# Optimization experiments

Hardware: AMD Instinct MI355X
Metric: run time of the kernel (lower is better)

The kernel has to match this reference:

```python
import jax, jax.numpy as jnp
import numpy as np

HEADS = 4
DIM_HEAD = 64


def setup_inputs() -> dict:
    key = jax.random.key(0)
    k1, k2, k3, k4 = jax.random.split(key, 4)
    dim = 256
    hidden = HEADS * DIM_HEAD  # 256
    x = jax.random.normal(k1, (16, dim, 64, 64), dtype=jnp.float32)
    # 1x1 conv weights stored as [out_c, in_c]
    w_qkv = jax.random.normal(k2, (3 * hidden, dim), dtype=jnp.float32) * (1.0 / np.sqrt(dim))
    w_out = jax.random.normal(k3, (dim, hidden), dtype=jnp.float32) * (1.0 / np.sqrt(hidden))
    b_out = jax.random.normal(k4, (dim,), dtype=jnp.float32) * 0.01
    gamma = jnp.ones((dim,), dtype=jnp.float32) * 1e-05
    return {"x": x, "w_qkv": w_qkv, "w_out": w_out, "b_out": b_out, "gamma": gamma}


def reference(x, w_qkv, w_out, b_out, gamma):
    b, c, h, w = x.shape
    n = h * w
    # 1x1 conv == channel matmul
    qkv = jnp.einsum('oc,bchw->bohw', w_qkv, x)  # [b, 3*heads*dh, h, w]
    qkv = qkv.reshape(b, 3, HEADS, DIM_HEAD, n)  # channel split order: (qkv, heads, c)
    q, k, v = qkv[:, 0], qkv[:, 1], qkv[:, 2]    # each [b, heads, dh, n]
    k = jax.nn.softmax(k, axis=-1)               # softmax over spatial tokens
    context = jnp.einsum('bhdn,bhen->bhde', k, v)  # [b, heads, dh, dh]
    out = jnp.einsum('bhde,bhdn->bhen', context, q)  # [b, heads, dh, n]
    out = out.reshape(b, HEADS * DIM_HEAD, h, w)
    y = jnp.einsum('oc,bchw->bohw', w_out, out) + b_out[None, :, None, None]
    return y * gamma[None, :, None, None] + x
```

## Files before the change

kernel.cpp:

```cpp
#include <hip/hip_runtime.h>
#include <stdint.h>

typedef short s16x8 __attribute__((ext_vector_type(8)));
typedef float f32x4 __attribute__((ext_vector_type(4)));
typedef unsigned int u32x2 __attribute__((ext_vector_type(2)));

typedef const __attribute__((address_space(1))) void glb_cv;
typedef __attribute__((address_space(3))) void lds_v;

__device__ __forceinline__ float bits2f(unsigned short u) {
    union { unsigned int i; float f; } c; c.i = ((unsigned int)u) << 16; return c.f;
}
__device__ __forceinline__ unsigned short f2bits(float f) {
    union { float f; unsigned int i; } c; c.f = f;
    unsigned int x = c.i;
    unsigned int r = (x + 0x7FFFu + ((x >> 16) & 1u)) >> 16;
    return (unsigned short)r;
}
__device__ __forceinline__ unsigned int pack2(float a, float b) {
    return (unsigned int)f2bits(a) | ((unsigned int)f2bits(b) << 16);
}

__device__ __forceinline__ void gl_lds16(const void* g, void* l) {
    __builtin_amdgcn_global_load_lds((glb_cv*)g, (lds_v*)l, 16, 0, 0);
}

__global__ __launch_bounds__(256) void k_cvt(
    const float* __restrict__ src, unsigned short* __restrict__ dst, int n8)
{
    int i = blockIdx.x * 256 + threadIdx.x;
    if (i >= n8) return;
    const float* s = src + (size_t)i * 8;
    float4 a = *(const float4*)s, b = *(const float4*)(s + 4);
    unsigned int q[4] = { pack2(a.x, a.y), pack2(a.z, a.w), pack2(b.x, b.y), pack2(b.z, b.w) };
    *(s16x8*)(dst + (size_t)i * 8) = *(s16x8*)q;
}

__global__ __launch_bounds__(256) void k_transpose(
    const unsigned short* __restrict__ src, unsigned short* __restrict__ dst,
    int RS, int DS)
{
    int dr = blockIdx.x * 256 + threadIdx.x;
    int c0 = blockIdx.y * 8;
    __align__(16) unsigned short tmp[8];
#pragma unroll
    for (int j = 0; j < 8; ++j) tmp[j] = src[(size_t)(c0 + j) * RS + dr];
    *(s16x8*)(dst + (size_t)dr * DS + c0) = *(s16x8*)tmp;
}

__global__ __launch_bounds__(256) void k_prepw(
    const float* __restrict__ wqkv, const float* __restrict__ wout,
    unsigned short* __restrict__ wb, unsigned short* __restrict__ wob,
    unsigned short* __restrict__ WqT)
{
    int i = blockIdx.x * 256 + threadIdx.x;
    if (i < 32768) {
        const float* s; unsigned short* d; int j;
        if (i < 24576) { s = wqkv; d = wb; j = i; }
        else           { s = wout; d = wob; j = i - 24576; }
        const float* sp = s + (size_t)j * 8;
        float4 a = *(const float4*)sp, b = *(const float4*)(sp + 4);
        unsigned int q[4] = { pack2(a.x, a.y), pack2(a.z, a.w), pack2(b.x, b.y), pack2(b.z, b.w) };
        *(s16x8*)(d + (size_t)j * 8) = *(s16x8*)q;
    } else {
        int j = i - 32768;
        int dr = j & 255, c0 = (j >> 8) * 8;
        __align__(16) unsigned short tmp[8];
#pragma unroll
        for (int jj = 0; jj < 8; ++jj)
            tmp[jj] = f2bits(wqkv[(size_t)(c0 + jj) * 256 + dr]);
        *(s16x8*)(WqT + (size_t)dr * 256 + c0) = *(s16x8*)tmp;
    }
}

__global__ __launch_bounds__(256) void k_prep(
    const float* __restrict__ x, unsigned short* __restrict__ xT,
    unsigned short* __restrict__ xbf)
{
    __shared__ unsigned short Ts[64][264];
    int b = blockIdx.y, n0 = blockIdx.x * 64, t = threadIdx.x;
    const float* xb = x + (size_t)b * 1048576;
    unsigned short* xbfb = xbf + (size_t)b * 1048576;
#pragma unroll
    for (int i = 0; i < 16; ++i) {
        int idx = t + i * 256;
        int c = idx >> 4, nq = idx & 15;
        float4 v = *(const float4*)(xb + (size_t)c * 4096 + n0 + nq * 4);
        u32x2 q; q[0] = pack2(v.x, v.y); q[1] = pack2(v.z, v.w);
        *(u32x2*)(xbfb + (size_t)c * 4096 + n0 + nq * 4) = q;
        float vv[4] = { v.x, v.y, v.z, v.w };
#pragma unroll
        for (int e = 0; e < 4; ++e) {
            int ee = (e + c) & 3;
            Ts[nq * 4 + ee][c] = f2bits(vv[ee]);
        }
    }
    __syncthreads();
    unsigned short* xTb = xT + (size_t)b * 1048576 + (size_t)n0 * 256;
#pragma unroll
    for (int i = 0; i < 8; ++i) {
        int idx = t + i * 256;
        int nl = idx >> 5, cg = (idx & 31) * 8;
        *(s16x8*)(xTb + (size_t)nl * 256 + cg) = *(const s16x8*)&Ts[nl][cg];
    }
}

template <int EPI>
__global__ __launch_bounds__(256) void gemm_bt2(
    const unsigned short* __restrict__ A, const unsigned short* __restrict__ Bt,
    void* __restrict__ C,
    int K, int Kstep, int lda, int ldb, int ldc,
    long Abs, long Bbs, long Cbs,
    const float* __restrict__ Xres,
    const float* __restrict__ gamma,
    const float* __restrict__ bias)
{
    __shared__ __align__(16) unsigned short As[128 * 64];
    __shared__ __align__(16) unsigned short Bs[128 * 64];
    int bz = blockIdx.z;
    int b = bz & 15, kc = bz >> 4;
    int m0 = blockIdx.y * 128, n0 = blockIdx.x * 128;
    const unsigned short* Ab = A + (size_t)b * Abs + (size_t)m0 * lda + (size_t)kc * Kstep;
    const unsigned short* Bb = Bt + (size_t)b * Bbs + (size_t)n0 * ldb + (size_t)kc * Kstep;
    int t = threadIdx.x;
    int w = t >> 6, l = t & 63, lm = l & 15, lq = l >> 4;
    int mw = (w >> 1) * 64, nw = (w & 1) * 64;

    f32x4 acc[4][4];
    f32x4 zero = {0.f, 0.f, 0.f, 0.f};
#pragma unroll
    for (int i = 0; i < 4; ++i)
#pragma unroll
        for (int j = 0; j < 4; ++j) acc[i][j] = zero;

    for (int kk = 0; kk < K; kk += 64) {
#pragma unroll
        for (int i = 0; i < 4; ++i) {
            int idx = t + i * 256;
            int r = idx >> 3;
            int sch = (idx & 7) ^ (r & 7);
            int lbase = (i * 256 + w * 64) * 8;
            gl_lds16(Ab + (size_t)r * lda + kk + sch * 8, &As[lbase]);
            gl_lds16(Bb + (size_t)r * ldb + kk + sch * 8, &Bs[lbase]);
        }
        __syncthreads();
#pragma unroll
        for (int ks = 0; ks < 2; ++ks) {
            s16x8 af[4], bfr[4];
#pragma unroll
            for (int mi = 0; mi < 4; ++mi) {
                int row = mw + mi * 16 + lm;
                af[mi] = *(const s16x8*)&As[row * 64 + (((ks * 4 + lq) ^ (row & 7)) << 3)];
            }
#pragma unroll
            for (int ni = 0; ni < 4; ++ni) {
                int row = nw + ni * 16 + lm;
                bfr[ni] = *(const s16x8*)&Bs[row * 64 + (((ks * 4 + lq) ^ (row & 7)) << 3)];
            }
#pragma unroll
            for (int mi = 0; mi < 4; ++mi)
#pragma unroll
                for (int ni = 0; ni < 4; ++ni)
                    acc[mi][ni] = __builtin_amdgcn_mfma_f32_16x16x32_bf16(af[mi], bfr[ni], acc[mi][ni], 0, 0, 0);
        }
        __syncthreads();
    }

    if (EPI == 0) {
        unsigned short* Cb = (unsigned short*)C + (size_t)bz * Cbs;
#pragma unroll
        for (int mi = 0; mi < 4; ++mi)
#pragma unroll
            for (int r = 0; r < 4; ++r) {
                int m = m0 + mw + mi * 16 + lq * 4 + r;
#pragma unroll
                for (int ni = 0; ni < 4; ++ni) {
                    int n = n0 + nw + ni * 16 + lm;
                    Cb[(size_t)m * ldc + n] = f2bits(acc[mi][ni][r]);
                }
            }
    } else {
        float* Cb = (float*)C + (size_t)bz * Cbs;
        const float* Xb = Xres + (size_t)bz * Cbs;
#pragma unroll
        for (int mi = 0; mi < 4; ++mi)
#pragma unroll
            for (int r = 0; r < 4; ++r) {
                int m = m0 + mw + mi * 16 + lq * 4 + r;
                float g = gamma[m], bo = bias[m];
#pragma unroll
                for (int ni = 0; ni < 4; ++ni) {
                    int n = n0 + nw + ni * 16 + lm;
                    size_t idx = (size_t)m * ldc + n;
                    Cb[idx] = g * (acc[mi][ni][r] + bo) + Xb[idx];
                }
            }
    }
}

__global__ __launch_bounds__(256) void gemm64(
    const unsigned short* __restrict__ A, const unsigned short* __restrict__ Bt,
    unsigned short* __restrict__ C,
    int K, int Kstep, int lda, int ldb, int ldc,
    long Abs, long Bbs, long Cbs)
{
    __shared__ __align__(16) unsigned short As[64 * 64];
    __shared__ __align__(16) unsigned short Bs[64 * 64];
    int bz = blockIdx.z;
    int b = bz & 15, kc = bz >> 4;
    int m0 = blockIdx.y * 64, n0 = blockIdx.x * 64;
    const unsigned short* Ab = A + (size_t)b * Abs + (size_t)m0 * lda + (size_t)kc * Kstep;
    const unsigned short* Bb = Bt + (size_t)b * Bbs + (size_t)n0 * ldb + (size_t)kc * Kstep;
    int t = threadIdx.x;
    int w = t >> 6, l = t & 63, lm = l & 15, lq = l >> 4;
    int mw = (w >> 1) * 32, nw = (w & 1) * 32;

    f32x4 acc[2][2];
    f32x4 zero = {0.f, 0.f, 0.f, 0.f};
#pragma unroll
    for (int i = 0; i < 2; ++i)
#pragma unroll
        for (int j = 0; j < 2; ++j) acc[i][j] = zero;

    for (int kk = 0; kk < K; kk += 64) {
#pragma unroll
        for (int i = 0; i < 2; ++i) {
            int idx = t + i * 256;
            int r = idx >> 3;
            int sch = (idx & 7) ^ (r & 7);
            int lbase = (i * 256 + w * 64) * 8;
            gl_lds16(Ab + (size_t)r * lda + kk + sch * 8, &As[lbase]);
            gl_lds16(Bb + (size_t)r * ldb + kk + sch * 8, &Bs[lbase]);
        }
        __syncthreads();
#pragma unroll
        for (int ks = 0; ks < 2; ++ks) {
            s16x8 af[2], bfr[2];
#pragma unroll
            for (int mi = 0; mi < 2; ++mi) {
                int row = mw + mi * 16 + lm;
                af[mi] = *(const s16x8*)&As[row * 64 + (((ks * 4 + lq) ^ (row & 7)) << 3)];
            }
#pragma unroll
            for (int ni = 0; ni < 2; ++ni) {
                int row = nw + ni * 16 + lm;
                bfr[ni] = *(const s16x8*)&Bs[row * 64 + (((ks * 4 + lq) ^ (row & 7)) << 3)];
            }
#pragma unroll
            for (int mi = 0; mi < 2; ++mi)
#pragma unroll
                for (int ni = 0; ni < 2; ++ni)
                    acc[mi][ni] = __builtin_amdgcn_mfma_f32_16x16x32_bf16(af[mi], bfr[ni], acc[mi][ni], 0, 0, 0);
        }
        __syncthreads();
    }

    unsigned short* Cb = C + (size_t)bz * Cbs;
#pragma unroll
    for (int mi = 0; mi < 2; ++mi)
#pragma unroll
        for (int r = 0; r < 4; ++r) {
            int m = m0 + mw + mi * 16 + lq * 4 + r;
#pragma unroll
            for (int ni = 0; ni < 2; ++ni) {
                int n = n0 + nw + ni * 16 + lm;
                Cb[(size_t)m * ldc + n] = f2bits(acc[mi][ni][r]);
            }
        }
}

template <int BF32, int EPI>
__global__ __launch_bounds__(256) void gemm_bt(
    const unsigned short* __restrict__ A, const void* __restrict__ Bt,
    void* __restrict__ C,
    int K, int Kstep, int lda, int ldb, int ldc,
    long Abs, long Bbs, long Cbs,
    const float* __restrict__ Xres,
    const float* __restrict__ gamma,
    const float* __restrict__ bias)
{
    __shared__ unsigned short As[128][72];
    __shared__ unsigned short Bs[128][72];
    int bz = blockIdx.z;
    int b = bz & 15, kc = bz >> 4;
    int m0 = blockIdx.y * 128, n0 = blockIdx.x * 128;
    const unsigned short* Ab = A + (size_t)b * Abs + (size_t)m0 * lda + (size_t)kc * Kstep;
    size_t boff = (size_t)b * Bbs + (size_t)n0 * ldb + (size_t)kc * Kstep;
    int t = threadIdx.x;
    int w = t >> 6, l = t & 63, lm = l & 15, lq = l >> 4;
    int mw = (w >> 1) * 64, nw = (w & 1) * 64;

    f32x4 acc[4][4];
    f32x4 zero = {0.f, 0.f, 0.f, 0.f};
#pragma unroll
    for (int i = 0; i < 4; ++i)
#pragma unroll
        for (int j = 0; j < 4; ++j) acc[i][j] = zero;

    for (int kk = 0; kk < K; kk += 64) {
#pragma unroll
        for (int i = 0; i < 4; ++i) {
            int idx = t + i * 256;
            int r = idx >> 3, ch = idx & 7;
            *(s16x8*)&As[r][ch * 8] = *(const s16x8*)(Ab + (size_t)r * lda + kk + ch * 8);
            if (BF32) {
                const float* bp = (const float*)Bt + boff + (size_t)r * ldb + kk + ch * 8;
                float4 v0 = *(const float4*)bp, v1 = *(const float4*)(bp + 4);
                unsigned int q[4] = { pack2(v0.x, v0.y), pack2(v0.z, v0.w),
                                      pack2(v1.x, v1.y), pack2(v1.z, v1.w) };
                *(s16x8*)&Bs[r][ch * 8] = *(s16x8*)q;
            } else {
                const unsigned short* bp = (const unsigned short*)Bt + boff + (size_t)r * ldb + kk + ch * 8;
                *(s16x8*)&Bs[r][ch * 8] = *(const s16x8*)bp;
            }
        }
        __syncthreads();
#pragma unroll
        for (int ks = 0; ks < 2; ++ks) {
            s16x8 af[4], bfr[4];
#pragma unroll
            for (int mi = 0; mi < 4; ++mi) af[mi]  = *(const s16x8*)&As[mw + mi * 16 + lm][ks * 32 + lq * 8];
#pragma unroll
            for (int ni = 0; ni < 4; ++ni) bfr[ni] = *(const s16x8*)&Bs[nw + ni * 16 + lm][ks * 32 + lq * 8];
#pragma unroll
            for (int mi = 0; mi < 4; ++mi)
#pragma unroll
                for (int ni = 0; ni < 4; ++ni)
                    acc[mi][ni] = __builtin_amdgcn_mfma_f32_16x16x32_bf16(af[mi], bfr[ni], acc[mi][ni], 0, 0, 0);
        }
        __syncthreads();
    }

    if (EPI == 0) {
        unsigned short* Cb = (unsigned short*)C + (size_t)bz * Cbs;
#pragma unroll
        for (int mi = 0; mi < 4; ++mi)
#pragma unroll
            for (int r = 0; r < 4; ++r) {
                int m = m0 + mw + mi * 16 + lq * 4 + r;
#pragma unroll
                for (int ni = 0; ni < 4; ++ni) {
                    int n = n0 + nw + ni * 16 + lm;
                    Cb[(size_t)m * ldc + n] = f2bits(acc[mi][ni][r]);
                }
            }
    } else {
        float* Cb = (float*)C + (size_t)bz * Cbs;
        const float* Xb = Xres + (size_t)bz * Cbs;
#pragma unroll
        for (int mi = 0; mi < 4; ++mi)
#pragma unroll
            for (int r = 0; r < 4; ++r) {
                int m = m0 + mw + mi * 16 + lq * 4 + r;
                float g = gamma[m], bo = bias[m];
#pragma unroll
                for (int ni = 0; ni < 4; ++ni) {
                    int n = n0 + nw + ni * 16 + lm;
                    size_t idx = (size_t)m * ldc + n;
                    Cb[idx] = g * (acc[mi][ni][r] + bo) + Xb[idx];
                }
            }
    }
}

template <int EPI>
__global__ __launch_bounds__(256) void gemm_bn(
    const unsigned short* __restrict__ A, const float* __restrict__ B,
    void* __restrict__ C,
    int K, int lda, int ldb, int ldc,
    long Abs, long Bbs, long Cbs,
    const float* __restrict__ Xres,
    const float* __restrict__ gamma,
    const float* __restrict__ bias)
{
    __shared__ unsigned short As[128][72];
    __shared__ unsigned short Bs[64][130];
    int bz = blockIdx.z;
    int m0 = blockIdx.y * 128, n0 = blockIdx.x * 128;
    const unsigned short* Ab = A + (size_t)bz * Abs + (size_t)m0 * lda;
    const float* Bb = B + (size_t)bz * Bbs + n0;
    int t = threadIdx.x;
    int w = t >> 6, l = t & 63, lm = l & 15, lq = l >> 4;
    int mw = (w >> 1) * 64, nw = (w & 1) * 64;

    f32x4 acc[4][4];
    f32x4 zero = {0.f, 0.f, 0.f, 0.f};
#pragma unroll
    for (int i = 0; i < 4; ++i)
#pragma unroll
        for (int j = 0; j < 4; ++j) acc[i][j] = zero;

    for (int kk = 0; kk < K; kk += 64) {
#pragma unroll
        for (int i = 0; i < 4; ++i) {
            int idx = t + i * 256;
            int r = idx >> 3, ch = idx & 7;
            *(s16x8*)&As[r][ch * 8] = *(const s16x8*)(Ab + (size_t)r * lda + kk + ch * 8);
        }
#pragma unroll
        for (int i = 0; i < 4; ++i) {
            int idx = t + i * 256;
            int c = idx >> 4, cc = idx & 15;
            const float* bp = Bb + (size_t)(kk + c) * ldb + cc * 8;
            float4 v0 = *(const float4*)bp, v1 = *(const float4*)(bp + 4);
            unsigned int* q = (unsigned int*)&Bs[c][cc * 8];
            q[0] = pack2(v0.x, v0.y); q[1] = pack2(v0.z, v0.w);
            q[2] = pack2(v1.x, v1.y); q[3] = pack2(v1.z, v1.w);
        }
        __syncthreads();
#pragma unroll
        for (int ks = 0; ks < 2; ++ks) {
            s16x8 af[4];
#pragma unroll
            for (int mi = 0; mi < 4; ++mi) af[mi] = *(const s16x8*)&As[mw + mi * 16 + lm][ks * 32 + lq * 8];
#pragma unroll
            for (int ni = 0; ni < 4; ++ni) {
                s16x8 bfr;
#pragma unroll
                for (int j = 0; j < 8; ++j) bfr[j] = (short)Bs[ks * 32 + lq * 8 + j][nw + ni * 16 + lm];
#pragma unroll
                for (int mi = 0; mi < 4; ++mi)
                    acc[mi][ni] = __builtin_amdgcn_mfma_f32_16x16x32_bf16(af[mi], bfr, acc[mi][ni], 0, 0, 0);
            }
        }
        __syncthreads();
    }

#pragma unroll
    for (int mi = 0; mi < 4; ++mi)
#pragma unroll
        for (int r = 0; r < 4; ++r) {
            int m = m0 + mw + mi * 16 + lq * 4 + r;
            float g = 0.f, bo = 0.f;
            if (EPI == 1) { g = gamma[m]; bo = bias[m]; }
#pragma unroll
            for (int ni = 0; ni < 4; ++ni) {
                int n = n0 + nw + ni * 16 + lm;
                size_t idx = (size_t)m * ldc + n;
                float v = acc[mi][ni][r];
                if (EPI == 1) {
                    float* Cb = (float*)C + (size_t)bz * Cbs;
                    Cb[idx] = g * (v + bo) + Xres[(size_t)bz * Cbs + idx];
                } else {
                    unsigned short* Cb = (unsigned short*)C + (size_t)bz * Cbs;
                    Cb[idx] = f2bits(v);
                }
            }
        }
}

__global__ __launch_bounds__(256) void k_softmax(unsigned short* __restrict__ kbuf)
{
    unsigned short* p = kbuf + (size_t)blockIdx.x * 4096;
    int t = threadIdx.x;
    __shared__ float red[4];

    s16x8 r0 = *(const s16x8*)(p + t * 16);
    s16x8 r1 = *(const s16x8*)(p + t * 16 + 8);
    float v[16];
    float m = -1e30f;
#pragma unroll
    for (int i = 0; i < 8; ++i) { v[i] = bits2f((unsigned short)r0[i]); v[8 + i] = bits2f((unsigned short)r1[i]); }
#pragma unroll
    for (int i = 0; i < 16; ++i) m = fmaxf(m, v[i]);
#pragma unroll
    for (int off = 32; off >= 1; off >>= 1) m = fmaxf(m, __shfl_xor(m, off));
    if ((t & 63) == 0) red[t >> 6] = m;
    __syncthreads();
    m = fmaxf(fmaxf(red[0], red[1]), fmaxf(red[2], red[3]));
    __syncthreads();

    float s = 0.f;
#pragma unroll
    for (int i = 0; i < 16; ++i) { v[i] = __expf(v[i] - m); s += v[i]; }
#pragma unroll
    for (int off = 32; off >= 1; off >>= 1) s += __shfl_xor(s, off);
    if ((t & 63) == 0) red[t >> 6] = s;
    __syncthreads();
    s = red[0] + red[1] + red[2] + red[3];
    float inv = 1.0f / s;

    __align__(16) unsigned short otmp[16];
#pragma unroll
    for (int i = 0; i < 16; ++i) otmp[i] = f2bits(v[i] * inv);
    *(s16x8*)(p + t * 16) = *(s16x8*)(otmp);
    *(s16x8*)(p + t * 16 + 8) = *(s16x8*)(otmp + 8);
}

template <int NC>
__global__ __launch_bounds__(256) void k_gred(
    const unsigned short* __restrict__ Gp, unsigned short* __restrict__ G)
{
    int gid = blockIdx.x * 256 + threadIdx.x;
    int b = gid >> 13;
    size_t i8 = (size_t)(gid & 8191) * 8;
    float s[8] = {0.f, 0.f, 0.f, 0.f, 0.f, 0.f, 0.f, 0.f};
#pragma unroll
    for (int kc = 0; kc < NC; ++kc) {
        s16x8 v = *(const s16x8*)(Gp + (size_t)(kc * 16 + b) * 65536 + i8);
#pragma unroll
        for (int j = 0; j < 8; ++j) s[j] += bits2f((unsigned short)v[j]);
    }
    __align__(16) unsigned short tmp[8];
#pragma unroll
    for (int j = 0; j < 8; ++j) tmp[j] = f2bits(s[j]);
    *(s16x8*)(G + (size_t)b * 65536 + i8) = *(s16x8*)tmp;
}

__global__ __launch_bounds__(256) void k_ctxw2(
    const unsigned short* __restrict__ G, const unsigned short* __restrict__ wb,
    const unsigned short* __restrict__ wob, unsigned short* __restrict__ W2)
{
    __shared__ unsigned short ctxs[64][72];
    int h = blockIdx.x, b = blockIdx.y;
    int t = threadIdx.x, w = t >> 6, l = t & 63, lm = l & 15, lq = l >> 4;
    const unsigned short* Gb = G + (size_t)b * 65536 + (size_t)(h * 64) * 256;
    const unsigned short* Wv = wb + 131072 + (size_t)(h * 64) * 256;
    f32x4 zero = {0.f, 0.f, 0.f, 0.f};

    f32x4 acc[4];
#pragma unroll
    for (int i = 0; i < 4; ++i) acc[i] = zero;
    for (int kk = 0; kk < 256; kk += 32) {
        s16x8 a = *(const s16x8*)(Gb + (size_t)(w * 16 + lm) * 256 + kk + lq * 8);
#pragma unroll
        for (int ni = 0; ni < 4; ++ni) {
            s16x8 bb = *(const s16x8*)(Wv + (size_t)(ni * 16 + lm) * 256 + kk + lq * 8);
            acc[ni] = __builtin_amdgcn_mfma_f32_16x16x32_bf16(a, bb, acc[ni], 0, 0, 0);
        }
    }
#pragma unroll
    for (int ni = 0; ni < 4; ++ni)
#pragma unroll
        for (int r = 0; r < 4; ++r)
            ctxs[w * 16 + lq * 4 + r][ni * 16 + lm] = f2bits(acc[ni][r]);
    __syncthreads();

    f32x4 acc2[4][4];
#pragma unroll
    for (int i = 0; i < 4; ++i)
#pragma unroll
        for (int j = 0; j < 4; ++j) acc2[i][j] = zero;
#pragma unroll
    for (int ks = 0; ks < 2; ++ks) {
        s16x8 af[4], bfr[4];
#pragma unroll
        for (int mi = 0; mi < 4; ++mi)
            af[mi] = *(const s16x8*)(wob + (size_t)(w * 64 + mi * 16 + lm) * 256 + h * 64 + ks * 32 + lq * 8);
#pragma unroll
        for (int ni = 0; ni < 4; ++ni) bfr[ni] = *(const s16x8*)&ctxs[ni * 16 + lm][ks * 32 + lq * 8];
#pragma unroll
        for (int mi = 0; mi < 4; ++mi)
#pragma unroll
            for (int ni = 0; ni < 4; ++ni)
                acc2[mi][ni] = __builtin_amdgcn_mfma_f32_16x16x32_bf16(af[mi], bfr[ni], acc2[mi][ni], 0, 0, 0);
    }
    unsigned short* W2b = W2 + (size_t)b * 65536;
#pragma unroll
    for (int mi = 0; mi < 4; ++mi)
#pragma unroll
        for (int r = 0; r < 4; ++r) {
            int o = w * 64 + mi * 16 + lq * 4 + r;
#pragma unroll
            for (int ni = 0; ni < 4; ++ni)
                W2b[(size_t)o * 256 + h * 64 + ni * 16 + lm] = f2bits(acc2[mi][ni][r]);
        }
}

extern "C" void kernel_launch(void* const* d_in, const int* in_sizes, int n_in,
                              void* d_out, int out_size, void* d_ws, size_t ws_size,
                              hipStream_t stream)
{
    (void)in_sizes; (void)n_in; (void)out_size;
    const float* x      = (const float*)d_in[0];
    const float* w_qkv  = (const float*)d_in[1];
    const float* w_out  = (const float*)d_in[2];
    const float* b_out  = (const float*)d_in[3];
    const float* gamma  = (const float*)d_in[4];

    char* ws = (char*)d_ws;
    const size_t NEED = 40501248;

    if (ws_size >= NEED) {
        unsigned short* xT  = (unsigned short*)ws;
        unsigned short* W3  = (unsigned short*)(ws + 33554432);
        unsigned short* Gp  = (unsigned short*)(ws + 35651584);
        unsigned short* WqT = (unsigned short*)(ws + 39845888);
        unsigned short* wb  = (unsigned short*)(ws + 39976960);
        unsigned short* wob = (unsigned short*)(ws + 40370176);
        unsigned short* kbuf = (unsigned short*)d_out;
        unsigned short* xbf  = (unsigned short*)d_out + 16777216;
        unsigned short* G    = (unsigned short*)d_out;
        unsigned short* W2   = (unsigned short*)d_out + 1048576;

        k_prepw<<<dim3(160), 256, 0, stream>>>(w_qkv, w_out, wb, wob, WqT);

        k_prep<<<dim3(64, 16), 256, 0, stream>>>(x, xT, xbf);

        gemm_bt2<0><<<dim3(32, 2, 16), 256, 0, stream>>>(
            wb + 65536, xT, kbuf, 256, 0, 256, 256, 4096,
            0L, 1048576L, 1048576L, nullptr, nullptr, nullptr);

        k_softmax<<<dim3(4096), 256, 0, stream>>>(kbuf);

        gemm64<<<dim3(4, 4, 32), 256, 0, stream>>>(
            kbuf, xbf, Gp, 2048, 2048, 4096, 4096, 256,
            1048576L, 1048576L, 65536L);

        k_gred<2><<<dim3(512), 256, 0, stream>>>(Gp, G);

        k_ctxw2<<<dim3(4, 16), 256, 0, stream>>>(G, wb, wob, W2);

        gemm64<<<dim3(4, 4, 16), 256, 0, stream>>>(
            W2, WqT, W3, 256, 0, 256, 256, 256,
            65536L, 0L, 65536L);

        gemm_bt2<1><<<dim3(32, 2, 16), 256, 0, stream>>>(
            W3, xT, d_out, 256, 0, 256, 256, 4096,
            65536L, 1048576L, 1048576L, x, gamma, b_out);
    } else {
        unsigned short* kbuf = (unsigned short*)d_out;
        unsigned short* Gp  = (unsigned short*)(ws);
        unsigned short* G   = (unsigned short*)(ws + 16777216);
        unsigned short* W2  = (unsigned short*)(ws + 18874368);
        unsigned short* W3  = (unsigned short*)(ws + 20971520);
        unsigned short* WqT = (unsigned short*)(ws + 23068672);
        unsigned short* wb  = (unsigned short*)(ws + 23199744);
        unsigned short* wob = (unsigned short*)(ws + 23592960);

        k_cvt<<<dim3(96), 256, 0, stream>>>(w_qkv, wb, 24576);
        k_cvt<<<dim3(32), 256, 0, stream>>>(w_out, wob, 8192);
        k_transpose<<<dim3(1, 32, 1), 256, 0, stream>>>(wb, WqT, 256, 256);

        gemm_bn<0><<<dim3(32, 2, 16), 256, 0, stream>>>(
            wb + 65536, x, kbuf, 256, 256, 4096, 4096,
            0L, 1048576L, 1048576L, nullptr, nullptr, nullptr);

        k_softmax<<<dim3(4096), 256, 0, stream>>>(kbuf);

        gemm_bt<1, 0><<<dim3(2, 2, 128), 256, 0, stream>>>(
            kbuf, x, Gp, 512, 512, 4096, 4096, 256,
            1048576L, 1048576L, 65536L, nullptr, nullptr, nullptr);

        k_gred<8><<<dim3(512), 256, 0, stream>>>(Gp, G);
        k_ctxw2<<<dim3(4, 16), 256, 0, stream>>>(G, wb, wob, W2);

        gemm_bt<0, 0><<<dim3(2, 2, 16), 256, 0, stream>>>(
            W2, WqT, W3, 256, 0, 256, 256, 256,
            65536L, 0L, 65536L, nullptr, nullptr, nullptr);

        gemm_bn<1><<<dim3(32, 2, 16), 256, 0, stream>>>(
            W3, x, d_out, 256, 256, 4096, 4096,
            65536L, 1048576L, 1048576L, x, gamma, b_out);
    }
}
```

Measured before the change: 230.0 us.

## Drop LDS staging in GEMMs, merge weight prep, fold split-K reduce into ctx kernel

Replaces the LDS-staged GEMMs (gemm_bt2, gemm64) with gemm_nl, which loads MFMA fragments straight from global memory with a compile-time K and no barriers. The weight conversion kernel is merged into k_prep as an extra grid row. The separate split-K reduction kernel is removed, and k_ctxw2g now sums the four partial Gram slices itself. The K·V GEMM switches to 4-way split-K with 128x128 tiles, and the workspace grows. This cuts launches and sync overhead, but each wave now reads operands from global memory without reuse through shared memory, so it depends on the cache to absorb the repeated loads.

```diff
diff --git a/kernel.cpp b/kernel.cpp
--- a/kernel.cpp
+++ b/kernel.cpp
@@ -4,9 +4,6 @@
 typedef short s16x8 __attribute__((ext_vector_type(8)));
 typedef float f32x4 __attribute__((ext_vector_type(4)));
 typedef unsigned int u32x2 __attribute__((ext_vector_type(2)));
-
-typedef const __attribute__((address_space(1))) void glb_cv;
-typedef __attribute__((address_space(3))) void lds_v;
 
 __device__ __forceinline__ float bits2f(unsigned short u) {
     union { unsigned int i; float f; } c; c.i = ((unsigned int)u) << 16; return c.f;
@@ -19,10 +16,6 @@
 }
 __device__ __forceinline__ unsigned int pack2(float a, float b) {
     return (unsigned int)f2bits(a) | ((unsigned int)f2bits(b) << 16);
-}
-
-__device__ __forceinline__ void gl_lds16(const void* g, void* l) {
-    __builtin_amdgcn_global_load_lds((glb_cv*)g, (lds_v*)l, 16, 0, 0);
 }
 
 __global__ __launch_bounds__(256) void k_cvt(
@@ -48,37 +41,42 @@
     *(s16x8*)(dst + (size_t)dr * DS + c0) = *(s16x8*)tmp;
 }
 
-__global__ __launch_bounds__(256) void k_prepw(
+__global__ __launch_bounds__(256) void k_prep(
+    const float* __restrict__ x, unsigned short* __restrict__ xT,
+    unsigned short* __restrict__ xbf,
     const float* __restrict__ wqkv, const float* __restrict__ wout,
     unsigned short* __restrict__ wb, unsigned short* __restrict__ wob,
     unsigned short* __restrict__ WqT)
 {
-    int i = blockIdx.x * 256 + threadIdx.x;
-    if (i < 32768) {
-        const float* s; unsigned short* d; int j;
-        if (i < 24576) { s = wqkv; d = wb; j = i; }
-        else           { s = wout; d = wob; j = i - 24576; }
-        const float* sp = s + (size_t)j * 8;
-        float4 a = *(const float4*)sp, b = *(const float4*)(sp + 4);
-        unsigned int q[4] = { pack2(a.x, a.y), pack2(a.z, a.w), pack2(b.x, b.y), pack2(b.z, b.w) };
-        *(s16x8*)(d + (size_t)j * 8) = *(s16x8*)q;
-    } else {
-        int j = i - 32768;
-        int dr = j & 255, c0 = (j >> 8) * 8;
-        __align__(16) unsigned short tmp[8];
-#pragma unroll
-        for (int jj = 0; jj < 8; ++jj)
-            tmp[jj] = f2bits(wqkv[(size_t)(c0 + jj) * 256 + dr]);
-        *(s16x8*)(WqT + (size_t)dr * 256 + c0) = *(s16x8*)tmp;
-    }
-}
-
-__global__ __launch_bounds__(256) void k_prep(
-    const float* __restrict__ x, unsigned short* __restrict__ xT,
-    unsigned short* __restrict__ xbf)
-{
+    int t = threadIdx.x;
+    if (blockIdx.y == 16) {
+#pragma unroll
+        for (int it = 0; it < 3; ++it) {
+            int i = blockIdx.x * 256 + t + it * 16384;
+            if (i >= 40960) break;
+            if (i < 32768) {
+                const float* s; unsigned short* d; int j;
+                if (i < 24576) { s = wqkv; d = wb; j = i; }
+                else           { s = wout; d = wob; j = i - 24576; }
+                const float* sp = s + (size_t)j * 8;
+                float4 a = *(const float4*)sp, b2 = *(const float4*)(sp + 4);
+                unsigned int q[4] = { pack2(a.x, a.y), pack2(a.z, a.w),
+                                      pack2(b2.x, b2.y), pack2(b2.z, b2.w) };
+                *(s16x8*)(d + (size_t)j * 8) = *(s16x8*)q;
+            } else {
+                int j = i - 32768;
+                int dr = j & 255, c0 = (j >> 8) * 8;
+                __align__(16) unsigned short tmp[8];
+#pragma unroll
+                for (int jj = 0; jj < 8; ++jj)
+                    tmp[jj] = f2bits(wqkv[(size_t)(c0 + jj) * 256 + dr]);
+                *(s16x8*)(WqT + (size_t)dr * 256 + c0) = *(s16x8*)tmp;
+            }
+        }
+        return;
+    }
     __shared__ unsigned short Ts[64][264];
-    int b = blockIdx.y, n0 = blockIdx.x * 64, t = threadIdx.x;
+    int b = blockIdx.y, n0 = blockIdx.x * 64;
     const float* xb = x + (size_t)b * 1048576;
     unsigned short* xbfb = xbf + (size_t)b * 1048576;
 #pragma unroll
@@ -105,27 +103,28 @@
     }
 }
 
-template <int EPI>
-__global__ __launch_bounds__(256) void gemm_bt2(
+template <int EPI, int KK>
+__global__ __launch_bounds__(256) void gemm_nl(
     const unsigned short* __restrict__ A, const unsigned short* __restrict__ Bt,
     void* __restrict__ C,
-    int K, int Kstep, int lda, int ldb, int ldc,
+    int lda, int ldb, int ldc,
     long Abs, long Bbs, long Cbs,
     const float* __restrict__ Xres,
     const float* __restrict__ gamma,
     const float* __restrict__ bias)
 {
-    __shared__ __align__(16) unsigned short As[128 * 64];
-    __shared__ __align__(16) unsigned short Bs[128 * 64];
     int bz = blockIdx.z;
     int b = bz & 15, kc = bz >> 4;
     int m0 = blockIdx.y * 128, n0 = blockIdx.x * 128;
-    const unsigned short* Ab = A + (size_t)b * Abs + (size_t)m0 * lda + (size_t)kc * Kstep;
-    const unsigned short* Bb = Bt + (size_t)b * Bbs + (size_t)n0 * ldb + (size_t)kc * Kstep;
     int t = threadIdx.x;
     int w = t >> 6, l = t & 63, lm = l & 15, lq = l >> 4;
     int mw = (w >> 1) * 64, nw = (w & 1) * 64;
 
+    const unsigned short* Ap = A + (size_t)b * Abs + (size_t)kc * KK
+                             + (size_t)(m0 + mw + lm) * lda + lq * 8;
+    const unsigned short* Bp = Bt + (size_t)b * Bbs + (size_t)kc * KK
+                             + (size_t)(n0 + nw + lm) * ldb + lq * 8;
+
     f32x4 acc[4][4];
     f32x4 zero = {0.f, 0.f, 0.f, 0.f};
 #pragma unroll
@@ -133,37 +132,20 @@
 #pragma unroll
         for (int j = 0; j < 4; ++j) acc[i][j] = zero;
 
-    for (int kk = 0; kk < K; kk += 64) {
-#pragma unroll
-        for (int i = 0; i < 4; ++i) {
-            int idx = t + i * 256;
-            int r = idx >> 3;
-            int sch = (idx & 7) ^ (r & 7);
-            int lbase = (i * 256 + w * 64) * 8;
-            gl_lds16(Ab + (size_t)r * lda + kk + sch * 8, &As[lbase]);
-            gl_lds16(Bb + (size_t)r * ldb + kk + sch * 8, &Bs[lbase]);
-        }
-        __syncthreads();
-#pragma unroll
-        for (int ks = 0; ks < 2; ++ks) {
-            s16x8 af[4], bfr[4];
-#pragma unroll
-            for (int mi = 0; mi < 4; ++mi) {
-                int row = mw + mi * 16 + lm;
-                af[mi] = *(const s16x8*)&As[row * 64 + (((ks * 4 + lq) ^ (row & 7)) << 3)];
-            }
-#pragma unroll
-            for (int ni = 0; ni < 4; ++ni) {
-                int row = nw + ni * 16 + lm;
-                bfr[ni] = *(const s16x8*)&Bs[row * 64 + (((ks * 4 + lq) ^ (row & 7)) << 3)];
-            }
-#pragma unroll
-            for (int mi = 0; mi < 4; ++mi)
-#pragma unroll
-                for (int ni = 0; ni < 4; ++ni)
-                    acc[mi][ni] = __builtin_amdgcn_mfma_f32_16x16x32_bf16(af[mi], bfr[ni], acc[mi][ni], 0, 0, 0);
-        }
-        __syncthreads();
+#pragma unroll 4
+    for (int kk = 0; kk < KK; kk += 32) {
+        s16x8 af[4], bfr[4];
+#pragma unroll
+        for (int mi = 0; mi < 4; ++mi)
+            af[mi] = *(const s16x8*)(Ap + (size_t)(mi * 16) * lda + kk);
+#pragma unroll
+        for (int ni = 0; ni < 4; ++ni)
+            bfr[ni] = *(const s16x8*)(Bp + (size_t)(ni * 16) * ldb + kk);
+#pragma unroll
+        for (int mi = 0; mi < 4; ++mi)
+#pragma unroll
+            for (int ni = 0; ni < 4; ++ni)
+                acc[mi][ni] = __builtin_amdgcn_mfma_f32_16x16x32_bf16(af[mi], bfr[ni], acc[mi][ni], 0, 0, 0);
     }
 
     if (EPI == 0) {
@@ -196,77 +178,6 @@
                 }
             }
     }
-}
-
-__global__ __launch_bounds__(256) void gemm64(
-    const unsigned short* __restrict__ A, const unsigned short* __restrict__ Bt,
-    unsigned short* __restrict__ C,
-    int K, int Kstep, int lda, int ldb, int ldc,
-    long Abs, long Bbs, long Cbs)
-{
-    __shared__ __align__(16) unsigned short As[64 * 64];
-    __shared__ __align__(16) unsigned short Bs[64 * 64];
-    int bz = blockIdx.z;
-    int b = bz & 15, kc = bz >> 4;
-    int m0 = blockIdx.y * 64, n0 = blockIdx.x * 64;
-    const unsigned short* Ab = A + (size_t)b * Abs + (size_t)m0 * lda + (size_t)kc * Kstep;
-    const unsigned short* Bb = Bt + (size_t)b * Bbs + (size_t)n0 * ldb + (size_t)kc * Kstep;
-    int t = threadIdx.x;
-    int w = t >> 6, l = t & 63, lm = l & 15, lq = l >> 4;
-    int mw = (w >> 1) * 32, nw = (w & 1) * 32;
-
-    f32x4 acc[2][2];
-    f32x4 zero = {0.f, 0.f, 0.f, 0.f};
-#pragma unroll
-    for (int i = 0; i < 2; ++i)
-#pragma unroll
-        for (int j = 0; j < 2; ++j) acc[i][j] = zero;
-
-    for (int kk = 0; kk < K; kk += 64) {
-#pragma unroll
-        for (int i = 0; i < 2; ++i) {
-            int idx = t + i * 256;
-            int r = idx >> 3;
-            int sch = (idx & 7) ^ (r & 7);
-            int lbase = (i * 256 + w * 64) * 8;
-            gl_lds16(Ab + (size_t)r * lda + kk + sch * 8, &As[lbase]);
-            gl_lds16(Bb + (size_t)r * ldb + kk + sch * 8, &Bs[lbase]);
-        }
-        __syncthreads();
-#pragma unroll
-        for (int ks = 0; ks < 2; ++ks) {
-            s16x8 af[2], bfr[2];
-#pragma unroll
-            for (int mi = 0; mi < 2; ++mi) {
-                int row = mw + mi * 16 + lm;
-                af[mi] = *(const s16x8*)&As[row * 64 + (((ks * 4 + lq) ^ (row & 7)) << 3)];
-            }
-#pragma unroll
-            for (int ni = 0; ni < 2; ++ni) {
-                int row = nw + ni * 16 + lm;
-                bfr[ni] = *(const s16x8*)&Bs[row * 64 + (((ks * 4 + lq) ^ (row & 7)) << 3)];
-            }
-#pragma unroll
-            for (int mi = 0; mi < 2; ++mi)
-#pragma unroll
-                for (int ni = 0; ni < 2; ++ni)
-                    acc[mi][ni] = __builtin_amdgcn_mfma_f32_16x16x32_bf16(af[mi], bfr[ni], acc[mi][ni], 0, 0, 0);
-        }
-        __syncthreads();
-    }
-
-    unsigned short* Cb = C + (size_t)bz * Cbs;
-#pragma unroll
-    for (int mi = 0; mi < 2; ++mi)
-#pragma unroll
-        for (int r = 0; r < 4; ++r) {
-            int m = m0 + mw + mi * 16 + lq * 4 + r;
-#pragma unroll
-            for (int ni = 0; ni < 2; ++ni) {
-                int n = n0 + nw + ni * 16 + lm;
-                Cb[(size_t)m * ldc + n] = f2bits(acc[mi][ni][r]);
-            }
-        }
 }
 
 template <int BF32, int EPI>
@@ -507,6 +418,69 @@
     *(s16x8*)(G + (size_t)b * 65536 + i8) = *(s16x8*)tmp;
 }
 
+__global__ __launch_bounds__(256) void k_ctxw2g(
+    const unsigned short* __restrict__ Gp, const unsigned short* __restrict__ wb,
+    const unsigned short* __restrict__ wob, unsigned short* __restrict__ W2)
+{
+    __shared__ unsigned short ctxs[64][72];
+    int h = blockIdx.x, b = blockIdx.y;
+    int t = threadIdx.x, w = t >> 6, l = t & 63, lm = l & 15, lq = l >> 4;
+    const unsigned short* Wv = wb + 131072 + (size_t)(h * 64) * 256;
+    f32x4 zero = {0.f, 0.f, 0.f, 0.f};
+
+    f32x4 acc[4];
+#pragma unroll
+    for (int i = 0; i < 4; ++i) acc[i] = zero;
+#pragma unroll
+    for (int kc = 0; kc < 4; ++kc) {
+        const unsigned short* Gb = Gp + (size_t)(kc * 16 + b) * 65536 + (size_t)(h * 64) * 256;
+        for (int kk = 0; kk < 256; kk += 32) {
+            s16x8 a = *(const s16x8*)(Gb + (size_t)(w * 16 + lm) * 256 + kk + lq * 8);
+#pragma unroll
+            for (int ni = 0; ni < 4; ++ni) {
+                s16x8 bb = *(const s16x8*)(Wv + (size_t)(ni * 16 + lm) * 256 + kk + lq * 8);
+                acc[ni] = __builtin_amdgcn_mfma_f32_16x16x32_bf16(a, bb, acc[ni], 0, 0, 0);
+            }
+        }
+    }
+#pragma unroll
+    for (int ni = 0; ni < 4; ++ni)
+#pragma unroll
+        for (int r = 0; r < 4; ++r)
+            ctxs[w * 16 + lq * 4 + r][ni * 16 + lm] = f2bits(acc[ni][r]);
+    __syncthreads();
+
+    f32x4 acc2[4][4];
+#pragma unroll
+    for (int i = 0; i < 4; ++i)
+#pragma unroll
+        for (int j = 0; j < 4; ++j) acc2[i][j] = zero;
+#pragma unroll
+    for (int ks = 0; ks < 2; ++ks) {
+        s16x8 af[4], bfr[4];
+#pragma unroll
+        for (int mi = 0; mi < 4; ++mi)
+            af[mi] = *(const s16x8*)(wob + (size_t)(w * 64 + mi * 16 + lm) * 256 + h * 64 + ks * 32 + lq * 8);
+#pragma unroll
+        for (int ni = 0; ni < 4; ++ni) bfr[ni] = *(const s16x8*)&ctxs[ni * 16 + lm][ks * 32 + lq * 8];
+#pragma unroll
+        for (int mi = 0; mi < 4; ++mi)
+#pragma unroll
+            for (int ni = 0; ni < 4; ++ni)
+                acc2[mi][ni] = __builtin_amdgcn_mfma_f32_16x16x32_bf16(af[mi], bfr[ni], acc2[mi][ni], 0, 0, 0);
+    }
+    unsigned short* W2b = W2 + (size_t)b * 65536;
+#pragma unroll
+    for (int mi = 0; mi < 4; ++mi)
+#pragma unroll
+        for (int r = 0; r < 4; ++r) {
+            int o = w * 64 + mi * 16 + lq * 4 + r;
+#pragma unroll
+            for (int ni = 0; ni < 4; ++ni)
+                W2b[(size_t)o * 256 + h * 64 + ni * 16 + lm] = f2bits(acc2[mi][ni][r]);
+        }
+}
+
 __global__ __launch_bounds__(256) void k_ctxw2(
     const unsigned short* __restrict__ G, const unsigned short* __restrict__ wb,
     const unsigned short* __restrict__ wob, unsigned short* __restrict__ W2)
@@ -579,44 +553,39 @@
     const float* gamma  = (const float*)d_in[4];
 
     char* ws = (char*)d_ws;
-    const size_t NEED = 40501248;
+    const size_t NEED = 44695552;
 
     if (ws_size >= NEED) {
         unsigned short* xT  = (unsigned short*)ws;
         unsigned short* W3  = (unsigned short*)(ws + 33554432);
         unsigned short* Gp  = (unsigned short*)(ws + 35651584);
-        unsigned short* WqT = (unsigned short*)(ws + 39845888);
-        unsigned short* wb  = (unsigned short*)(ws + 39976960);
-        unsigned short* wob = (unsigned short*)(ws + 40370176);
+        unsigned short* WqT = (unsigned short*)(ws + 44040192);
+        unsigned short* wb  = (unsigned short*)(ws + 44171264);
+        unsigned short* wob = (unsigned short*)(ws + 44564480);
         unsigned short* kbuf = (unsigned short*)d_out;
         unsigned short* xbf  = (unsigned short*)d_out + 16777216;
-        unsigned short* G    = (unsigned short*)d_out;
         unsigned short* W2   = (unsigned short*)d_out + 1048576;
 
-        k_prepw<<<dim3(160), 256, 0, stream>>>(w_qkv, w_out, wb, wob, WqT);
-
-        k_prep<<<dim3(64, 16), 256, 0, stream>>>(x, xT, xbf);
-
-        gemm_bt2<0><<<dim3(32, 2, 16), 256, 0, stream>>>(
-            wb + 65536, xT, kbuf, 256, 0, 256, 256, 4096,
+        k_prep<<<dim3(64, 17), 256, 0, stream>>>(x, xT, xbf, w_qkv, w_out, wb, wob, WqT);
+
+        gemm_nl<0, 256><<<dim3(32, 2, 16), 256, 0, stream>>>(
+            wb + 65536, xT, kbuf, 256, 256, 4096,
             0L, 1048576L, 1048576L, nullptr, nullptr, nullptr);
 
         k_softmax<<<dim3(4096), 256, 0, stream>>>(kbuf);
 
-        gemm64<<<dim3(4, 4, 32), 256, 0, stream>>>(
-            kbuf, xbf, Gp, 2048, 2048, 4096, 4096, 256,
-            1048576L, 1048576L, 65536L);
-
-        k_gred<2><<<dim3(512), 256, 0, stream>>>(Gp, G);
-
-        k_ctxw2<<<dim3(4, 16), 256, 0, stream>>>(G, wb, wob, W2);
-
-        gemm64<<<dim3(4, 4, 16), 256, 0, stream>>>(
-            W2, WqT, W3, 256, 0, 256, 256, 256,
-            65536L, 0L, 65536L);
-
-        gemm_bt2<1><<<dim3(32, 2, 16), 256, 0, stream>>>(
-            W3, xT, d_out, 256, 0, 256, 256, 4096,
+        gemm_nl<0, 1024><<<dim3(2, 2, 64), 256, 0, stream>>>(
+            kbuf, xbf, Gp, 4096, 4096, 256,
+            1048576L, 1048576L, 65536L, nullptr, nullptr, nullptr);
+
+        k_ctxw2g<<<dim3(4, 16), 256, 0, stream>>>(Gp, wb, wob, W2);
+
+        gemm_nl<0, 256><<<dim3(2, 2, 16), 256, 0, stream>>>(
+            W2, WqT, W3, 256, 256, 256,
+            65536L, 0L, 65536L, nullptr, nullptr, nullptr);
+
+        gemm_nl<1, 256><<<dim3(32, 2, 16), 256, 0, stream>>>(
+            W3, xT, d_out, 256, 256, 4096,
             65536L, 1048576L, 1048576L, x, gamma, b_out);
     } else {
         unsigned short* kbuf = (unsigned short*)d_out;
```

After: 277.3 us. 1.21x slower.
